# Optimization experiments

Hardware: AMD Instinct MI355X
Metric: run time of the kernel (lower is better)

## Reference

```python
import jax, jax.numpy as jnp
import numpy as np

D_MODEL = 1024
NUM_HEADS = 16
HEAD_DIM = D_MODEL // NUM_HEADS  # 64
B, S = 4, 2048


def setup_inputs() -> dict:
    key = jax.random.key(0)
    ks = jax.random.split(key, 10)
    scale = 1.0 / np.sqrt(D_MODEL)
    x = jax.random.normal(ks[0], (B, S, D_MODEL), dtype=jnp.float32)
    # per-head projection weights stacked over the head axis (matches ModuleList of Linears)
    Wq = jax.random.normal(ks[1], (NUM_HEADS, D_MODEL, HEAD_DIM), dtype=jnp.float32) * scale
    bq = jax.random.normal(ks[2], (NUM_HEADS, HEAD_DIM), dtype=jnp.float32) * 0.01
    Wk = jax.random.normal(ks[3], (NUM_HEADS, D_MODEL, HEAD_DIM), dtype=jnp.float32) * scale
    bk = jax.random.normal(ks[4], (NUM_HEADS, HEAD_DIM), dtype=jnp.float32) * 0.01
    Wv = jax.random.normal(ks[5], (NUM_HEADS, D_MODEL, HEAD_DIM), dtype=jnp.float32) * scale
    bv = jax.random.normal(ks[6], (NUM_HEADS, HEAD_DIM), dtype=jnp.float32) * 0.01
    Wo = jax.random.normal(ks[7], (D_MODEL, D_MODEL), dtype=jnp.float32) * scale
    bo = jax.random.normal(ks[8], (D_MODEL,), dtype=jnp.float32) * 0.01
    return {"hidden_state": x, "Wq": Wq, "bq": bq, "Wk": Wk, "bk": bk,
            "Wv": Wv, "bv": bv, "Wo": Wo, "bo": bo}


def reference(hidden_state, Wq, bq, Wk, bk, Wv, bv, Wo, bo):
    # q,k,v: [B, H, S, E]
    q = jnp.einsum('bsd,hde->bhse', hidden_state, Wq) + bq[None, :, None, :]
    k = jnp.einsum('bsd,hde->bhse', hidden_state, Wk) + bk[None, :, None, :]
    v = jnp.einsum('bsd,hde->bhse', hidden_state, Wv) + bv[None, :, None, :]
    scores = jnp.einsum('bhse,bhte->bhst', q, k) / jnp.sqrt(jnp.asarray(HEAD_DIM, q.dtype))
    weights = jax.nn.softmax(scores, axis=-1)  # [B, H, S, S]
    attn = jnp.einsum('bhst,bhte->bhse', weights, v)  # [B, H, S, E]
    # concat heads along feature dim (head order preserved)
    attn = jnp.transpose(attn, (0, 2, 1, 3)).reshape(hidden_state.shape[0], hidden_state.shape[1], D_MODEL)
    return attn @ Wo + bo
```

## Files before the change

kernel.cpp:

```cpp
#include <hip/hip_runtime.h>

typedef __bf16 bf16x8 __attribute__((ext_vector_type(8)));
typedef float f32x4 __attribute__((ext_vector_type(4)));
typedef unsigned int u32x4 __attribute__((ext_vector_type(4)));
typedef unsigned int u32x2 __attribute__((ext_vector_type(2)));
typedef unsigned short u16x8 __attribute__((ext_vector_type(8)));

#define MFMA_BF16(a, b, c) __builtin_amdgcn_mfma_f32_16x16x32_bf16((a), (b), (c), 0, 0, 0)

#define QSCALE 0.18033688011112043f

__device__ __forceinline__ unsigned short f2bf(float f) {
    unsigned int u = __builtin_bit_cast(unsigned int, f);
    u += 0x7FFFu + ((u >> 16) & 1u);
    return (unsigned short)(u >> 16);
}

__device__ __forceinline__ unsigned int pack_bf16_rne(float a, float b) {
    unsigned int ua = __builtin_bit_cast(unsigned int, a);
    unsigned int ub = __builtin_bit_cast(unsigned int, b);
    ua += 0x7FFFu + ((ua >> 16) & 1u);
    ub += 0x7FFFu + ((ub >> 16) & 1u);
    return __builtin_amdgcn_perm(ub, ua, 0x07060302);
}

#if __has_builtin(__builtin_amdgcn_cvt_pk_bf16_f32)
typedef __bf16 bf16x2 __attribute__((ext_vector_type(2)));
__device__ __forceinline__ unsigned int pack_bf16(float a, float b) {
    return __builtin_bit_cast(unsigned int, __builtin_amdgcn_cvt_pk_bf16_f32(a, b));
}
#else
__device__ __forceinline__ unsigned int pack_bf16(float a, float b) {
    return pack_bf16_rne(a, b);
}
#endif

#if __has_builtin(__builtin_amdgcn_exp2f)
__device__ __forceinline__ float fast_exp2(float x) { return __builtin_amdgcn_exp2f(x); }
#else
__device__ __forceinline__ float fast_exp2(float x) { return exp2f(x); }
#endif

__device__ __forceinline__ bf16x8 ldfrag(const unsigned short* p) {
    return __builtin_bit_cast(bf16x8, *(const u32x4*)p);
}

typedef const __attribute__((address_space(1))) void* gas_t;
typedef __attribute__((address_space(3))) void* las_t;
__device__ __forceinline__ void dma16(const unsigned short* g, unsigned short* l) {
    __builtin_amdgcn_global_load_lds((gas_t)(const void*)g, (las_t)(void*)l, 16, 0, 0);
}

__device__ __forceinline__ void pipeline_barrier() {
    __builtin_amdgcn_s_waitcnt(0);
    __syncthreads();
}


__global__ void cvt_x_kernel(const float* __restrict__ in, unsigned short* __restrict__ out) {
    long long t = (long long)blockIdx.x * 256 + threadIdx.x;
    const f32x4* p = (const f32x4*)in + t * 2;
    f32x4 v0 = p[0], v1 = p[1];
    u16x8 o;
    o[0] = f2bf(v0[0]); o[1] = f2bf(v0[1]); o[2] = f2bf(v0[2]); o[3] = f2bf(v0[3]);
    o[4] = f2bf(v1[0]); o[5] = f2bf(v1[1]); o[6] = f2bf(v1[2]); o[7] = f2bf(v1[3]);
    *((u16x8*)out + t) = o;
}

__global__ void cvt_wqkvT_kernel(const float* __restrict__ Wq, const float* __restrict__ Wk,
                                 const float* __restrict__ Wv, unsigned short* __restrict__ WT) {
    int n = blockIdx.x * 256 + threadIdx.x;
    int d0 = blockIdx.y * 8;
    int proj = n >> 10, rem = n & 1023, h = rem >> 6, e = rem & 63;
    const float* W = (proj == 0) ? Wq : (proj == 1) ? Wk : Wv;
    const float* src = W + (size_t)h * 65536 + (size_t)d0 * 64 + e;
    u16x8 o;
#pragma unroll
    for (int j = 0; j < 8; j++) o[j] = f2bf(src[j * 64]);
    *(u16x8*)(WT + (size_t)n * 1024 + d0) = o;
}

__global__ void cvt_woT_kernel(const float* __restrict__ Wo, unsigned short* __restrict__ WoT) {
    int n = blockIdx.x * 256 + threadIdx.x;
    int d0 = blockIdx.y * 8;
    const float* src = Wo + (size_t)d0 * 1024 + n;
    u16x8 o;
#pragma unroll
    for (int j = 0; j < 8; j++) o[j] = f2bf(src[j * 1024]);
    *(u16x8*)(WoT + (size_t)n * 1024 + d0) = o;
}


__global__ __launch_bounds__(256) void gemm_qkv_kernel(
    const unsigned short* __restrict__ A, const unsigned short* __restrict__ BT,
    const float* __restrict__ bq, const float* __restrict__ bk, const float* __restrict__ bv,
    unsigned short* __restrict__ Qo, unsigned short* __restrict__ Ko, unsigned short* __restrict__ VTo) {
    __shared__ unsigned short As[2 * 128 * 32];
    __shared__ unsigned short Bs[2 * 128 * 32];
    const int tid = threadIdx.x;
    const int m0 = blockIdx.y * 128, n0 = blockIdx.x * 128;
    const int w = tid >> 6, lane = tid & 63, lr = lane & 15, quad = lane >> 4;
    const int wy = w >> 1, wx = w & 1;
    f32x4 acc[4][4];
#pragma unroll
    for (int i = 0; i < 4; i++)
#pragma unroll
        for (int j = 0; j < 4; j++) acc[i][j] = (f32x4){0.f, 0.f, 0.f, 0.f};
    const int drow = lane >> 2;
    const int dchunk = (lane & 3) ^ (drow & 3);
    const unsigned short* gA = A + (size_t)(m0 + w * 32 + drow) * 1024 + dchunk * 8;
    const unsigned short* gB = BT + (size_t)(n0 + w * 32 + drow) * 1024 + dchunk * 8;
    const int swav = (w * 32) * 32;
    const int fcol = (quad ^ (lr & 3)) * 8;
    dma16(gA, As + swav);
    dma16(gA + 16 * 1024, As + swav + 16 * 32);
    dma16(gB, Bs + swav);
    dma16(gB + 16 * 1024, Bs + swav + 16 * 32);
    for (int k0 = 0; k0 < 1024; k0 += 32) {
        const int cur = (k0 >> 5) & 1;
        const unsigned short* cA = As + cur * 4096;
        const unsigned short* cB = Bs + cur * 4096;
        pipeline_barrier();
        bf16x8 af[4], bfr[4];
#pragma unroll
        for (int i = 0; i < 4; i++) af[i] = ldfrag(cA + (wy * 64 + i * 16 + lr) * 32 + fcol);
#pragma unroll
        for (int j = 0; j < 4; j++) bfr[j] = ldfrag(cB + (wx * 64 + j * 16 + lr) * 32 + fcol);
        if (k0 + 32 < 1024) {
            const int nb = (cur ^ 1) * 4096 + swav;
            dma16(gA + k0 + 32, As + nb);
            dma16(gA + k0 + 32 + 16 * 1024, As + nb + 16 * 32);
            dma16(gB + k0 + 32, Bs + nb);
            dma16(gB + k0 + 32 + 16 * 1024, Bs + nb + 16 * 32);
        }
#pragma unroll
        for (int i = 0; i < 4; i++)
#pragma unroll
            for (int j = 0; j < 4; j++) acc[i][j] = MFMA_BF16(af[i], bfr[j], acc[i][j]);
    }
#pragma unroll
    for (int j = 0; j < 4; j++) {
        int n = n0 + wx * 64 + j * 16 + lr;
        int proj = n >> 10, rem = n & 1023, h = rem >> 6, e = rem & 63;
        if (proj == 2) {
            float bb = bv[rem];
#pragma unroll
            for (int i = 0; i < 4; i++) {
                int m = m0 + wy * 64 + i * 16 + quad * 4;
                int batch = m >> 11, s = m & 2047;
                u32x2 pk;
                pk[0] = pack_bf16_rne(acc[i][j][0] + bb, acc[i][j][1] + bb);
                pk[1] = pack_bf16_rne(acc[i][j][2] + bb, acc[i][j][3] + bb);
                *(u32x2*)(VTo + (((size_t)batch * 16 + h) * 64 + e) * 2048 + s) = pk;
            }
        } else {
            const float* bias = (proj == 0) ? bq : bk;
            unsigned short* dst = (proj == 0) ? Qo : Ko;
            float bb = bias[rem];
            float scl = (proj == 0) ? QSCALE : 1.0f;
#pragma unroll
            for (int i = 0; i < 4; i++) {
#pragma unroll
                for (int r = 0; r < 4; r++) {
                    int m = m0 + wy * 64 + i * 16 + quad * 4 + r;
                    int batch = m >> 11, s = m & 2047;
                    dst[(((size_t)batch * 16 + h) * 2048 + s) * 64 + e] = f2bf((acc[i][j][r] + bb) * scl);
                }
            }
        }
    }
}

__global__ __launch_bounds__(256) void gemm_out_kernel(
    const unsigned short* __restrict__ A, const unsigned short* __restrict__ BT,
    const float* __restrict__ bo, float* __restrict__ out) {
    __shared__ unsigned short As[2 * 128 * 32];
    __shared__ unsigned short Bs[2 * 128 * 32];
    const int tid = threadIdx.x;
    const int m0 = blockIdx.y * 128, n0 = blockIdx.x * 128;
    const int w = tid >> 6, lane = tid & 63, lr = lane & 15, quad = lane >> 4;
    const int wy = w >> 1, wx = w & 1;
    f32x4 acc[4][4];
#pragma unroll
    for (int i = 0; i < 4; i++)
#pragma unroll
        for (int j = 0; j < 4; j++) acc[i][j] = (f32x4){0.f, 0.f, 0.f, 0.f};
    const int drow = lane >> 2;
    const int dchunk = (lane & 3) ^ (drow & 3);
    const unsigned short* gA = A + (size_t)(m0 + w * 32 + drow) * 1024 + dchunk * 8;
    const unsigned short* gB = BT + (size_t)(n0 + w * 32 + drow) * 1024 + dchunk * 8;
    const int swav = (w * 32) * 32;
    const int fcol = (quad ^ (lr & 3)) * 8;
    dma16(gA, As + swav);
    dma16(gA + 16 * 1024, As + swav + 16 * 32);
    dma16(gB, Bs + swav);
    dma16(gB + 16 * 1024, Bs + swav + 16 * 32);
    for (int k0 = 0; k0 < 1024; k0 += 32) {
        const int cur = (k0 >> 5) & 1;
        const unsigned short* cA = As + cur * 4096;
        const unsigned short* cB = Bs + cur * 4096;
        pipeline_barrier();
        bf16x8 af[4], bfr[4];
#pragma unroll
        for (int i = 0; i < 4; i++) af[i] = ldfrag(cA + (wy * 64 + i * 16 + lr) * 32 + fcol);
#pragma unroll
        for (int j = 0; j < 4; j++) bfr[j] = ldfrag(cB + (wx * 64 + j * 16 + lr) * 32 + fcol);
        if (k0 + 32 < 1024) {
            const int nb = (cur ^ 1) * 4096 + swav;
            dma16(gA + k0 + 32, As + nb);
            dma16(gA + k0 + 32 + 16 * 1024, As + nb + 16 * 32);
            dma16(gB + k0 + 32, Bs + nb);
            dma16(gB + k0 + 32 + 16 * 1024, Bs + nb + 16 * 32);
        }
#pragma unroll
        for (int i = 0; i < 4; i++)
#pragma unroll
            for (int j = 0; j < 4; j++) acc[i][j] = MFMA_BF16(af[i], bfr[j], acc[i][j]);
    }
#pragma unroll
    for (int j = 0; j < 4; j++) {
        int n = n0 + wx * 64 + j * 16 + lr;
        float bb = bo[n];
#pragma unroll
        for (int i = 0; i < 4; i++) {
#pragma unroll
            for (int r = 0; r < 4; r++) {
                int m = m0 + wy * 64 + i * 16 + quad * 4 + r;
                out[(size_t)m * 1024 + n] = acc[i][j][r] + bb;
            }
        }
    }
}

__global__ __launch_bounds__(256, 2) void attn_fa_kernel(
    const unsigned short* __restrict__ Q, const unsigned short* __restrict__ K,
    const unsigned short* __restrict__ VT, unsigned short* __restrict__ Out) {
    __shared__ unsigned short Ks[2 * 64 * 64];
    __shared__ unsigned short Vs[2 * 64 * 64];
    __shared__ unsigned short Ps[256 * 64];
    const int bh = blockIdx.x;
    const int q0 = blockIdx.y * 256;
    const int tid = threadIdx.x;
    const int w = tid >> 6, lane = tid & 63, lr = lane & 15, quad = lane >> 4;
    const unsigned short* Qh = Q + (size_t)bh * 2048 * 64;
    const unsigned short* Kh = K + (size_t)bh * 2048 * 64;
    const unsigned short* Vh = VT + (size_t)bh * 64 * 2048;

    const f32x4 ZERO4 = {0.f, 0.f, 0.f, 0.f};

    const int drow = lane >> 3;
    const int dchunk = (lane & 7) ^ drow;
    const unsigned short* gK = Kh + (size_t)(w * 16 + drow) * 64 + dchunk * 8;
    const unsigned short* gV = Vh + (size_t)(w * 16 + drow) * 2048 + dchunk * 8;
    const int swav = (w * 16) * 64;
    dma16(gK, Ks + swav);
    dma16(gK + 8 * 64, Ks + swav + 8 * 64);
    dma16(gV, Vs + swav);
    dma16(gV + 8 * 2048, Vs + swav + 8 * 64);

    bf16x8 qb[4][2];
#pragma unroll
    for (int nt = 0; nt < 4; nt++)
#pragma unroll
        for (int kc = 0; kc < 2; kc++)
            qb[nt][kc] = ldfrag(Qh + (size_t)(q0 + w * 64 + nt * 16 + lr) * 64 + kc * 32 + quad * 8);

    f32x4 o[4][4];
#pragma unroll
    for (int i = 0; i < 4; i++)
#pragma unroll
        for (int j = 0; j < 4; j++) o[i][j] = ZERO4;
    float lp[4] = {0.f, 0.f, 0.f, 0.f};

    unsigned short* const Pw = Ps + (w * 64) * 64;
    const int swzb = lr & 7;

    for (int t0 = 0; t0 < 2048; t0 += 64) {
        const int cur = (t0 >> 6) & 1;
        const unsigned short* cK = Ks + cur * 4096;
        const unsigned short* cV = Vs + cur * 4096;
        pipeline_barrier();
        bf16x8 ka[2][4];
#pragma unroll
        for (int kc = 0; kc < 2; kc++)
#pragma unroll
            for (int mt = 0; mt < 4; mt++)
                ka[kc][mt] = ldfrag(cK + (mt * 16 + lr) * 64 + ((kc * 4 + quad) ^ swzb) * 8);
        if (t0 + 64 < 2048) {
            const int nb = (cur ^ 1) * 4096 + swav;
            dma16(gK + (size_t)(t0 + 64) * 64, Ks + nb);
            dma16(gK + (size_t)(t0 + 64) * 64 + 8 * 64, Ks + nb + 8 * 64);
            dma16(gV + t0 + 64, Vs + nb);
            dma16(gV + t0 + 64 + 8 * 2048, Vs + nb + 8 * 64);
        }

#pragma unroll
        for (int mt = 0; mt < 4; mt++) {
            f32x4 sc[4];
#pragma unroll
            for (int nt = 0; nt < 4; nt++) {
                f32x4 z = ZERO4;
                sc[nt] = MFMA_BF16(ka[0][mt], qb[nt][0], z);
                sc[nt] = MFMA_BF16(ka[1][mt], qb[nt][1], sc[nt]);
            }
#pragma unroll
            for (int nt = 0; nt < 4; nt++) {
                float p0 = fast_exp2(sc[nt][0]);
                float p1 = fast_exp2(sc[nt][1]);
                float p2 = fast_exp2(sc[nt][2]);
                float p3 = fast_exp2(sc[nt][3]);
                lp[nt] += (p0 + p1) + (p2 + p3);
                u32x2 pk;
                pk[0] = pack_bf16(p0, p1);
                pk[1] = pack_bf16(p2, p3);
                *(u32x2*)(Pw + (nt * 16 + lr) * 64 + ((2 * mt + (quad >> 1)) ^ swzb) * 8 +
                          (quad & 1) * 4) = pk;
            }
        }

#pragma unroll
        for (int kc = 0; kc < 2; kc++) {
            const int fc = ((kc * 4 + quad) ^ swzb) * 8;
            bf16x8 vb[4];
#pragma unroll
            for (int et = 0; et < 4; et++) vb[et] = ldfrag(cV + (et * 16 + lr) * 64 + fc);
#pragma unroll
            for (int g = 0; g < 4; g++) {
                bf16x8 pa = ldfrag(Pw + (g * 16 + lr) * 64 + fc);
                o[g][0] = MFMA_BF16(pa, vb[0], o[g][0]);
                o[g][1] = MFMA_BF16(pa, vb[1], o[g][1]);
                o[g][2] = MFMA_BF16(pa, vb[2], o[g][2]);
                o[g][3] = MFMA_BF16(pa, vb[3], o[g][3]);
            }
        }
    }

#pragma unroll
    for (int g = 0; g < 4; g++) {
        float l = lp[g];
        l += __shfl_xor(l, 16, 64);
        l += __shfl_xor(l, 32, 64);
        lp[g] = l;
    }

    const int h = bh & 15, b = bh >> 4;
#pragma unroll
    for (int g = 0; g < 4; g++) {
#pragma unroll
        for (int r = 0; r < 4; r++) {
            float l = __shfl(lp[g], quad * 4 + r, 16);
            float inv = 1.0f / l;
            int s = q0 + w * 64 + g * 16 + quad * 4 + r;
#pragma unroll
            for (int et = 0; et < 4; et++) {
                int col = h * 64 + et * 16 + lr;
                Out[((size_t)(b * 2048 + s)) * 1024 + col] = f2bf(o[g][et][r] * inv);
            }
        }
    }
}


extern "C" void kernel_launch(void* const* d_in, const int* in_sizes, int n_in,
                              void* d_out, int out_size, void* d_ws, size_t ws_size,
                              hipStream_t stream) {
    const float* x  = (const float*)d_in[0];
    const float* Wq = (const float*)d_in[1];
    const float* bq = (const float*)d_in[2];
    const float* Wk = (const float*)d_in[3];
    const float* bk = (const float*)d_in[4];
    const float* Wv = (const float*)d_in[5];
    const float* bv = (const float*)d_in[6];
    const float* Wo = (const float*)d_in[7];
    const float* bo = (const float*)d_in[8];
    float* out = (float*)d_out;

    char* ws = (char*)d_ws;
    unsigned short* xb    = (unsigned short*)(ws);
    unsigned short* WqkvT = (unsigned short*)(ws + 16777216);
    unsigned short* WoT   = (unsigned short*)(ws + 23068672);
    unsigned short* Qb    = (unsigned short*)(ws + 25165824);
    unsigned short* Kb    = (unsigned short*)(ws + 41943040);
    unsigned short* VTb   = (unsigned short*)(ws + 58720256);
    unsigned short* attn  = xb;

    cvt_x_kernel<<<dim3(4096), dim3(256), 0, stream>>>(x, xb);
    cvt_wqkvT_kernel<<<dim3(12, 128), dim3(256), 0, stream>>>(Wq, Wk, Wv, WqkvT);
    cvt_woT_kernel<<<dim3(4, 128), dim3(256), 0, stream>>>(Wo, WoT);
    gemm_qkv_kernel<<<dim3(24, 64), dim3(256), 0, stream>>>(xb, WqkvT, bq, bk, bv, Qb, Kb, VTb);
    attn_fa_kernel<<<dim3(64, 8), dim3(256), 0, stream>>>(Qb, Kb, VTb, attn);
    gemm_out_kernel<<<dim3(8, 64), dim3(256), 0, stream>>>(attn, WoT, bo, out);
}
```

Baseline: 281.8 us.

## Load K/V fragments directly from global memory instead of LDS double buffering

Result: slower. 324.1 us (+15.0%).

```diff
diff --git a/kernel.cpp b/kernel.cpp
--- a/kernel.cpp
+++ b/kernel.cpp
@@ -232,11 +232,9 @@
     }
 }
 
-__global__ __launch_bounds__(256, 2) void attn_fa_kernel(
+__global__ __launch_bounds__(256) void attn_fa_kernel(
     const unsigned short* __restrict__ Q, const unsigned short* __restrict__ K,
     const unsigned short* __restrict__ VT, unsigned short* __restrict__ Out) {
-    __shared__ unsigned short Ks[2 * 64 * 64];
-    __shared__ unsigned short Vs[2 * 64 * 64];
     __shared__ unsigned short Ps[256 * 64];
     const int bh = blockIdx.x;
     const int q0 = blockIdx.y * 256;
@@ -248,16 +246,6 @@
 
     const f32x4 ZERO4 = {0.f, 0.f, 0.f, 0.f};
 
-    const int drow = lane >> 3;
-    const int dchunk = (lane & 7) ^ drow;
-    const unsigned short* gK = Kh + (size_t)(w * 16 + drow) * 64 + dchunk * 8;
-    const unsigned short* gV = Vh + (size_t)(w * 16 + drow) * 2048 + dchunk * 8;
-    const int swav = (w * 16) * 64;
-    dma16(gK, Ks + swav);
-    dma16(gK + 8 * 64, Ks + swav + 8 * 64);
-    dma16(gV, Vs + swav);
-    dma16(gV + 8 * 2048, Vs + swav + 8 * 64);
-
     bf16x8 qb[4][2];
 #pragma unroll
     for (int nt = 0; nt < 4; nt++)
@@ -275,34 +263,28 @@
     unsigned short* const Pw = Ps + (w * 64) * 64;
     const int swzb = lr & 7;
 
+    const unsigned short* const Kfb = Kh + (size_t)lr * 64 + quad * 8;
+    const unsigned short* const Vfb = Vh + (size_t)lr * 2048 + quad * 8;
+
     for (int t0 = 0; t0 < 2048; t0 += 64) {
-        const int cur = (t0 >> 6) & 1;
-        const unsigned short* cK = Ks + cur * 4096;
-        const unsigned short* cV = Vs + cur * 4096;
-        pipeline_barrier();
         bf16x8 ka[2][4];
 #pragma unroll
         for (int kc = 0; kc < 2; kc++)
 #pragma unroll
             for (int mt = 0; mt < 4; mt++)
-                ka[kc][mt] = ldfrag(cK + (mt * 16 + lr) * 64 + ((kc * 4 + quad) ^ swzb) * 8);
-        if (t0 + 64 < 2048) {
-            const int nb = (cur ^ 1) * 4096 + swav;
-            dma16(gK + (size_t)(t0 + 64) * 64, Ks + nb);
-            dma16(gK + (size_t)(t0 + 64) * 64 + 8 * 64, Ks + nb + 8 * 64);
-            dma16(gV + t0 + 64, Vs + nb);
-            dma16(gV + t0 + 64 + 8 * 2048, Vs + nb + 8 * 64);
-        }
+                ka[kc][mt] = ldfrag(Kfb + (size_t)(t0 + mt * 16) * 64 + kc * 32);
 
 #pragma unroll
         for (int mt = 0; mt < 4; mt++) {
             f32x4 sc[4];
+            __builtin_amdgcn_s_setprio(1);
 #pragma unroll
             for (int nt = 0; nt < 4; nt++) {
                 f32x4 z = ZERO4;
                 sc[nt] = MFMA_BF16(ka[0][mt], qb[nt][0], z);
                 sc[nt] = MFMA_BF16(ka[1][mt], qb[nt][1], sc[nt]);
             }
+            __builtin_amdgcn_s_setprio(0);
 #pragma unroll
             for (int nt = 0; nt < 4; nt++) {
                 float p0 = fast_exp2(sc[nt][0]);
@@ -323,15 +305,20 @@
             const int fc = ((kc * 4 + quad) ^ swzb) * 8;
             bf16x8 vb[4];
 #pragma unroll
-            for (int et = 0; et < 4; et++) vb[et] = ldfrag(cV + (et * 16 + lr) * 64 + fc);
+            for (int et = 0; et < 4; et++)
+                vb[et] = ldfrag(Vfb + (size_t)(et * 16) * 2048 + t0 + kc * 32);
+            bf16x8 pa[4];
+#pragma unroll
+            for (int g = 0; g < 4; g++) pa[g] = ldfrag(Pw + (g * 16 + lr) * 64 + fc);
+            __builtin_amdgcn_s_setprio(1);
 #pragma unroll
             for (int g = 0; g < 4; g++) {
-                bf16x8 pa = ldfrag(Pw + (g * 16 + lr) * 64 + fc);
-                o[g][0] = MFMA_BF16(pa, vb[0], o[g][0]);
-                o[g][1] = MFMA_BF16(pa, vb[1], o[g][1]);
-                o[g][2] = MFMA_BF16(pa, vb[2], o[g][2]);
-                o[g][3] = MFMA_BF16(pa, vb[3], o[g][3]);
-            }
+                o[g][0] = MFMA_BF16(pa[g], vb[0], o[g][0]);
+                o[g][1] = MFMA_BF16(pa[g], vb[1], o[g][1]);
+                o[g][2] = MFMA_BF16(pa[g], vb[2], o[g][2]);
+                o[g][3] = MFMA_BF16(pa[g], vb[3], o[g][3]);
+            }
+            __builtin_amdgcn_s_setprio(0);
         }
     }
 
```

## Load V fragments directly from global memory and raise MFMA wave priority

Applied to the files above, without the earlier changes.

After: 290.9 us. 3.2% more time.

```diff
diff --git a/kernel.cpp b/kernel.cpp
--- a/kernel.cpp
+++ b/kernel.cpp
@@ -236,7 +236,6 @@
     const unsigned short* __restrict__ Q, const unsigned short* __restrict__ K,
     const unsigned short* __restrict__ VT, unsigned short* __restrict__ Out) {
     __shared__ unsigned short Ks[2 * 64 * 64];
-    __shared__ unsigned short Vs[2 * 64 * 64];
     __shared__ unsigned short Ps[256 * 64];
     const int bh = blockIdx.x;
     const int q0 = blockIdx.y * 256;
@@ -251,12 +250,9 @@
     const int drow = lane >> 3;
     const int dchunk = (lane & 7) ^ drow;
     const unsigned short* gK = Kh + (size_t)(w * 16 + drow) * 64 + dchunk * 8;
-    const unsigned short* gV = Vh + (size_t)(w * 16 + drow) * 2048 + dchunk * 8;
     const int swav = (w * 16) * 64;
     dma16(gK, Ks + swav);
     dma16(gK + 8 * 64, Ks + swav + 8 * 64);
-    dma16(gV, Vs + swav);
-    dma16(gV + 8 * 2048, Vs + swav + 8 * 64);
 
     bf16x8 qb[4][2];
 #pragma unroll
@@ -274,35 +270,45 @@
 
     unsigned short* const Pw = Ps + (w * 64) * 64;
     const int swzb = lr & 7;
+
+    const unsigned short* const Vfb = Vh + (size_t)lr * 2048 + quad * 8;
 
     for (int t0 = 0; t0 < 2048; t0 += 64) {
         const int cur = (t0 >> 6) & 1;
         const unsigned short* cK = Ks + cur * 4096;
-        const unsigned short* cV = Vs + cur * 4096;
         pipeline_barrier();
+
+        bf16x8 vb[2][4];
+#pragma unroll
+        for (int kc = 0; kc < 2; kc++)
+#pragma unroll
+            for (int et = 0; et < 4; et++)
+                vb[kc][et] = ldfrag(Vfb + (size_t)(et * 16) * 2048 + t0 + kc * 32);
+
         bf16x8 ka[2][4];
 #pragma unroll
         for (int kc = 0; kc < 2; kc++)
 #pragma unroll
             for (int mt = 0; mt < 4; mt++)
                 ka[kc][mt] = ldfrag(cK + (mt * 16 + lr) * 64 + ((kc * 4 + quad) ^ swzb) * 8);
+
         if (t0 + 64 < 2048) {
             const int nb = (cur ^ 1) * 4096 + swav;
             dma16(gK + (size_t)(t0 + 64) * 64, Ks + nb);
             dma16(gK + (size_t)(t0 + 64) * 64 + 8 * 64, Ks + nb + 8 * 64);
-            dma16(gV + t0 + 64, Vs + nb);
-            dma16(gV + t0 + 64 + 8 * 2048, Vs + nb + 8 * 64);
         }
 
 #pragma unroll
         for (int mt = 0; mt < 4; mt++) {
             f32x4 sc[4];
+            __builtin_amdgcn_s_setprio(1);
 #pragma unroll
             for (int nt = 0; nt < 4; nt++) {
                 f32x4 z = ZERO4;
                 sc[nt] = MFMA_BF16(ka[0][mt], qb[nt][0], z);
                 sc[nt] = MFMA_BF16(ka[1][mt], qb[nt][1], sc[nt]);
             }
+            __builtin_amdgcn_s_setprio(0);
 #pragma unroll
             for (int nt = 0; nt < 4; nt++) {
                 float p0 = fast_exp2(sc[nt][0]);
@@ -321,17 +327,18 @@
 #pragma unroll
         for (int kc = 0; kc < 2; kc++) {
             const int fc = ((kc * 4 + quad) ^ swzb) * 8;
-            bf16x8 vb[4];
-#pragma unroll
-            for (int et = 0; et < 4; et++) vb[et] = ldfrag(cV + (et * 16 + lr) * 64 + fc);
+            bf16x8 pa[4];
+#pragma unroll
+            for (int g = 0; g < 4; g++) pa[g] = ldfrag(Pw + (g * 16 + lr) * 64 + fc);
+            __builtin_amdgcn_s_setprio(1);
 #pragma unroll
             for (int g = 0; g < 4; g++) {
-                bf16x8 pa = ldfrag(Pw + (g * 16 + lr) * 64 + fc);
-                o[g][0] = MFMA_BF16(pa, vb[0], o[g][0]);
-                o[g][1] = MFMA_BF16(pa, vb[1], o[g][1]);
-                o[g][2] = MFMA_BF16(pa, vb[2], o[g][2]);
-                o[g][3] = MFMA_BF16(pa, vb[3], o[g][3]);
-            }
+                o[g][0] = MFMA_BF16(pa[g], vb[kc][0], o[g][0]);
+                o[g][1] = MFMA_BF16(pa[g], vb[kc][1], o[g][1]);
+                o[g][2] = MFMA_BF16(pa[g], vb[kc][2], o[g][2]);
+                o[g][3] = MFMA_BF16(pa[g], vb[kc][3], o[g][3]);
+            }
+            __builtin_amdgcn_s_setprio(0);
         }
     }
 
```

## Software-pipeline attention PV with next QK^T; XCD-aware block remap for GEMMs

Applied to the files above, without the earlier changes.

After: 307.5 us. 1.09x slower.

```diff
diff --git a/kernel.cpp b/kernel.cpp
--- a/kernel.cpp
+++ b/kernel.cpp
@@ -98,7 +98,9 @@
     __shared__ unsigned short As[2 * 128 * 32];
     __shared__ unsigned short Bs[2 * 128 * 32];
     const int tid = threadIdx.x;
-    const int m0 = blockIdx.y * 128, n0 = blockIdx.x * 128;
+    const int bid = blockIdx.x;
+    const int sid = (bid & 7) * 192 + (bid >> 3);
+    const int m0 = (sid / 24) * 128, n0 = (sid % 24) * 128;
     const int w = tid >> 6, lane = tid & 63, lr = lane & 15, quad = lane >> 4;
     const int wy = w >> 1, wx = w & 1;
     f32x4 acc[4][4];
@@ -177,7 +179,9 @@
     __shared__ unsigned short As[2 * 128 * 32];
     __shared__ unsigned short Bs[2 * 128 * 32];
     const int tid = threadIdx.x;
-    const int m0 = blockIdx.y * 128, n0 = blockIdx.x * 128;
+    const int bid = blockIdx.x;
+    const int sid = (bid & 7) * 64 + (bid >> 3);
+    const int m0 = (sid >> 3) * 128, n0 = (sid & 7) * 128;
     const int w = tid >> 6, lane = tid & 63, lr = lane & 15, quad = lane >> 4;
     const int wy = w >> 1, wx = w & 1;
     f32x4 acc[4][4];
@@ -275,25 +279,16 @@
     unsigned short* const Pw = Ps + (w * 64) * 64;
     const int swzb = lr & 7;
 
-    for (int t0 = 0; t0 < 2048; t0 += 64) {
-        const int cur = (t0 >> 6) & 1;
-        const unsigned short* cK = Ks + cur * 4096;
-        const unsigned short* cV = Vs + cur * 4096;
-        pipeline_barrier();
+    bf16x8 vbp[2][4];
+    bf16x8 pap[2][4];
+
+    auto qkt_softmax = [&](const unsigned short* cK) {
         bf16x8 ka[2][4];
 #pragma unroll
         for (int kc = 0; kc < 2; kc++)
 #pragma unroll
             for (int mt = 0; mt < 4; mt++)
                 ka[kc][mt] = ldfrag(cK + (mt * 16 + lr) * 64 + ((kc * 4 + quad) ^ swzb) * 8);
-        if (t0 + 64 < 2048) {
-            const int nb = (cur ^ 1) * 4096 + swav;
-            dma16(gK + (size_t)(t0 + 64) * 64, Ks + nb);
-            dma16(gK + (size_t)(t0 + 64) * 64 + 8 * 64, Ks + nb + 8 * 64);
-            dma16(gV + t0 + 64, Vs + nb);
-            dma16(gV + t0 + 64 + 8 * 2048, Vs + nb + 8 * 64);
-        }
-
 #pragma unroll
         for (int mt = 0; mt < 4; mt++) {
             f32x4 sc[4];
@@ -317,23 +312,65 @@
                           (quad & 1) * 4) = pk;
             }
         }
-
+    };
+    auto read_pa = [&]() {
 #pragma unroll
         for (int kc = 0; kc < 2; kc++) {
             const int fc = ((kc * 4 + quad) ^ swzb) * 8;
-            bf16x8 vb[4];
-#pragma unroll
-            for (int et = 0; et < 4; et++) vb[et] = ldfrag(cV + (et * 16 + lr) * 64 + fc);
+#pragma unroll
+            for (int g = 0; g < 4; g++) pap[kc][g] = ldfrag(Pw + (g * 16 + lr) * 64 + fc);
+        }
+    };
+    auto read_vb = [&](const unsigned short* cV) {
+#pragma unroll
+        for (int kc = 0; kc < 2; kc++) {
+            const int fc = ((kc * 4 + quad) ^ swzb) * 8;
+#pragma unroll
+            for (int et = 0; et < 4; et++) vbp[kc][et] = ldfrag(cV + (et * 16 + lr) * 64 + fc);
+        }
+    };
+    auto do_pv = [&]() {
+#pragma unroll
+        for (int kc = 0; kc < 2; kc++)
 #pragma unroll
             for (int g = 0; g < 4; g++) {
-                bf16x8 pa = ldfrag(Pw + (g * 16 + lr) * 64 + fc);
-                o[g][0] = MFMA_BF16(pa, vb[0], o[g][0]);
-                o[g][1] = MFMA_BF16(pa, vb[1], o[g][1]);
-                o[g][2] = MFMA_BF16(pa, vb[2], o[g][2]);
-                o[g][3] = MFMA_BF16(pa, vb[3], o[g][3]);
-            }
-        }
-    }
+                o[g][0] = MFMA_BF16(pap[kc][g], vbp[kc][0], o[g][0]);
+                o[g][1] = MFMA_BF16(pap[kc][g], vbp[kc][1], o[g][1]);
+                o[g][2] = MFMA_BF16(pap[kc][g], vbp[kc][2], o[g][2]);
+                o[g][3] = MFMA_BF16(pap[kc][g], vbp[kc][3], o[g][3]);
+            }
+    };
+
+    pipeline_barrier();
+    {
+        const int nb = 4096 + swav;
+        dma16(gK + 64 * 64, Ks + nb);
+        dma16(gK + 64 * 64 + 8 * 64, Ks + nb + 8 * 64);
+        dma16(gV + 64, Vs + nb);
+        dma16(gV + 64 + 8 * 2048, Vs + nb + 8 * 64);
+        qkt_softmax(Ks);
+        read_vb(Vs);
+    }
+
+    for (int t0 = 64; t0 < 2048; t0 += 64) {
+        const int cur = (t0 >> 6) & 1;
+        const unsigned short* cK = Ks + cur * 4096;
+        const unsigned short* cV = Vs + cur * 4096;
+        pipeline_barrier();
+        read_pa();
+        if (t0 + 64 < 2048) {
+            const int nb = (cur ^ 1) * 4096 + swav;
+            dma16(gK + (size_t)(t0 + 64) * 64, Ks + nb);
+            dma16(gK + (size_t)(t0 + 64) * 64 + 8 * 64, Ks + nb + 8 * 64);
+            dma16(gV + t0 + 64, Vs + nb);
+            dma16(gV + t0 + 64 + 8 * 2048, Vs + nb + 8 * 64);
+        }
+        qkt_softmax(cK);
+        do_pv();
+        read_vb(cV);
+    }
+    read_pa();
+    do_pv();
 
 #pragma unroll
     for (int g = 0; g < 4; g++) {
@@ -387,7 +424,7 @@
     cvt_x_kernel<<<dim3(4096), dim3(256), 0, stream>>>(x, xb);
     cvt_wqkvT_kernel<<<dim3(12, 128), dim3(256), 0, stream>>>(Wq, Wk, Wv, WqkvT);
     cvt_woT_kernel<<<dim3(4, 128), dim3(256), 0, stream>>>(Wo, WoT);
-    gemm_qkv_kernel<<<dim3(24, 64), dim3(256), 0, stream>>>(xb, WqkvT, bq, bk, bv, Qb, Kb, VTb);
+    gemm_qkv_kernel<<<dim3(1536), dim3(256), 0, stream>>>(xb, WqkvT, bq, bk, bv, Qb, Kb, VTb);
     attn_fa_kernel<<<dim3(64, 8), dim3(256), 0, stream>>>(Qb, Kb, VTb, attn);
-    gemm_out_kernel<<<dim3(8, 64), dim3(256), 0, stream>>>(attn, WoT, bo, out);
-}
+    gemm_out_kernel<<<dim3(512), dim3(256), 0, stream>>>(attn, WoT, bo, out);
+}
```
